# Performance work log

Hardware: AMD Instinct MI355X
Metric: run time of the kernel (lower is better)

## Reference

```python
import jax, jax.numpy as jnp
import numpy as np
from jax import lax

EPS = 1e-5

def _dsconv(x, dw, pw, g, b, m, v, relu):
    # x: [B,C,H,W]; dw: [C,1,3,3] depthwise; pw: [C,C,1,1] pointwise; eval-mode BN
    C = x.shape[1]
    y = lax.conv_general_dilated(x, dw, (1, 1), 'SAME', feature_group_count=C)
    y = lax.conv_general_dilated(y, pw, (1, 1), 'SAME')
    scale = (g * lax.rsqrt(v + EPS))[None, :, None, None]
    y = y * scale + (b - m * g * lax.rsqrt(v + EPS))[None, :, None, None]
    return jnp.maximum(y, 0.0) if relu else y

def _attention(x, wq, bq, wk, bk, wv, bv, gamma):
    b, c, h, w = x.shape
    n = h * w
    xf = x.reshape(b, c, n)                      # [B,C,N]
    q = jnp.einsum('oc,bcn->bon', wq, xf) + bq[None, :, None]   # [B,C/8,N]
    k = jnp.einsum('oc,bcn->bon', wk, xf) + bk[None, :, None]   # [B,C/8,N]
    v = jnp.einsum('oc,bcn->bon', wv, xf) + bv[None, :, None]   # [B,C,N]
    logits = jnp.einsum('bdm,bdn->bmn', q, k)    # q^T k, [B,N,N]
    attn = jax.nn.softmax(logits, axis=2)
    out = jnp.einsum('bcn,bmn->bcm', v, attn).reshape(b, c, h, w)
    return gamma[0] * out + x

def setup_inputs() -> dict:
    key = jax.random.key(0)
    ks = jax.random.split(key, 20)
    B, C, H, W = 64, 256, 32, 32
    C8 = C // 8
    rn = lambda k, s, sc: (jax.random.normal(k, s, dtype=jnp.float32) * sc)
    return {
        'x': rn(ks[0], (B, C, H, W), 1.0),
        'dw1': rn(ks[1], (C, 1, 3, 3), 0.2),
        'pw1': rn(ks[2], (C, C, 1, 1), 0.06),
        'bn1_g': jax.random.uniform(ks[3], (C,), jnp.float32, 0.5, 1.5),
        'bn1_b': rn(ks[4], (C,), 0.1),
        'bn1_m': rn(ks[5], (C,), 0.1),
        'bn1_v': jax.random.uniform(ks[6], (C,), jnp.float32, 0.5, 1.5),
        'dw2': rn(ks[7], (C, 1, 3, 3), 0.2),
        'pw2': rn(ks[8], (C, C, 1, 1), 0.06),
        'bn2_g': jax.random.uniform(ks[9], (C,), jnp.float32, 0.5, 1.5),
        'bn2_b': rn(ks[10], (C,), 0.1),
        'bn2_m': rn(ks[11], (C,), 0.1),
        'bn2_v': jax.random.uniform(ks[12], (C,), jnp.float32, 0.5, 1.5),
        'wq': rn(ks[13], (C8, C), 0.06),
        'bq': rn(ks[14], (C8,), 0.02),
        'wk': rn(ks[15], (C8, C), 0.06),
        'bk': rn(ks[16], (C8,), 0.02),
        'wv': rn(ks[17], (C, C), 0.06),
        'bv': rn(ks[18], (C,), 0.02),
        'gamma': rn(ks[19], (1,), 0.5),
    }

def reference(x, dw1, pw1, bn1_g, bn1_b, bn1_m, bn1_v,
              dw2, pw2, bn2_g, bn2_b, bn2_m, bn2_v,
              wq, bq, wk, bk, wv, bv, gamma):
    out = _dsconv(x, dw1, pw1, bn1_g, bn1_b, bn1_m, bn1_v, relu=True)
    out = _dsconv(out, dw2, pw2, bn2_g, bn2_b, bn2_m, bn2_v, relu=False)
    out = _attention(out + x, wq, bq, wk, bk, wv, bv, gamma)
    return jnp.maximum(out, 0.0)
```

## Files before the change

kernel.cpp:

```cpp
#include <hip/hip_runtime.h>
#include <cstdint>
#include <cstddef>

#define B_ 64
#define C_ 256
#define N_ 1024
#define LOG2E 1.4426950408889634f

typedef short v8s __attribute__((ext_vector_type(8)));
typedef float v4f __attribute__((ext_vector_type(4)));
typedef unsigned int u32;
typedef unsigned short u16;

__device__ __forceinline__ float bf2f(u16 u) {
  return __uint_as_float(((u32)u) << 16);
}
__device__ __forceinline__ u16 f2bf(float f) {
  u32 x = __float_as_uint(f);
  x += 0x7fffu + ((x >> 16) & 1u);
  return (u16)(x >> 16);
}
__device__ __forceinline__ u32 pack2(float a, float b) {
  return (u32)f2bf(a) | ((u32)f2bf(b) << 16);
}

typedef __attribute__((address_space(3))) unsigned int lds_as_t;
typedef __attribute__((address_space(1))) const unsigned int glb_as_t;
__device__ __forceinline__ void ld_lds16(const u16* g, u16* l) {
  __builtin_amdgcn_global_load_lds((glb_as_t*)g, (lds_as_t*)l, 16, 0, 0);
}

__global__ __launch_bounds__(256) void prep(
    const float* __restrict__ g1, const float* __restrict__ b1,
    const float* __restrict__ m1, const float* __restrict__ v1,
    const float* __restrict__ g2, const float* __restrict__ b2,
    const float* __restrict__ m2, const float* __restrict__ v2,
    const float* __restrict__ wq, const float* __restrict__ bq,
    const float* __restrict__ wk, const float* __restrict__ bk,
    const float* __restrict__ wv, const float* __restrict__ bv,
    const float* __restrict__ pw1, const float* __restrict__ pw2,
    const float* __restrict__ dw1, const float* __restrict__ dw2,
    float* __restrict__ scale1, float* __restrict__ shift1,
    float* __restrict__ scale2, float* __restrict__ shift2,
    float* __restrict__ dwT1, float* __restrict__ dwT2,
    u16* __restrict__ pw1b, u16* __restrict__ pw2b, u16* __restrict__ wcatb,
    float* __restrict__ bcat) {
  const int gt = blockIdx.x * 256 + threadIdx.x;
  if (gt < 256) {
    float s1 = g1[gt] * rsqrtf(v1[gt] + 1e-5f);
    scale1[gt] = s1;
    shift1[gt] = b1[gt] - m1[gt] * s1;
    float s2 = g2[gt] * rsqrtf(v2[gt] + 1e-5f);
    scale2[gt] = s2;
    shift2[gt] = b2[gt] - m2[gt] * s2;
  }
  if (gt < 320)
    bcat[gt] = (gt < 32) ? bq[gt] * LOG2E
                         : (gt < 64) ? bk[gt - 32] : bv[gt - 64];
  if (gt < 2304) {
    dwT1[(gt % 9) * 256 + gt / 9] = dw1[gt];
    dwT2[(gt % 9) * 256 + gt / 9] = dw2[gt];
  }
  for (int e = gt; e < 65536; e += 16384) {
    pw1b[e] = f2bf(pw1[e]);
    pw2b[e] = f2bf(pw2[e]);
  }
  for (int e = gt; e < 81920; e += 16384) {
    const int o = e >> 8;
    float w = (o < 32) ? wq[e] * LOG2E
                       : (o < 64) ? wk[e - 8192] : wv[e - 16384];
    wcatb[e] = f2bf(w);
  }
}

__global__ __launch_bounds__(256) void transpose_x(const float* __restrict__ x,
                                                   u16* __restrict__ xt) {
  __shared__ float t[64][65];
  const int b = blockIdx.z, c0 = blockIdx.y * 64, n0 = blockIdx.x * 64;
  const float* xp = x + ((size_t)b * C_ + c0) * N_ + n0;
  const int tn = threadIdx.x & 63, tc = threadIdx.x >> 6;
#pragma unroll
  for (int i = 0; i < 16; ++i)
    t[tc + 4 * i][tn] = xp[(size_t)(tc + 4 * i) * N_ + tn];
  __syncthreads();
  u16* op = xt + ((size_t)b * N_ + n0) * C_ + c0;
  const int oc = threadIdx.x & 63, on = threadIdx.x >> 6;
#pragma unroll
  for (int i = 0; i < 16; ++i)
    op[(size_t)(on + 4 * i) * C_ + oc] = f2bf(t[oc][on + 4 * i]);
}

__global__ __launch_bounds__(256) void dw_nhwc(const u16* __restrict__ src,
                                               const float* __restrict__ wT,
                                               u16* __restrict__ dst) {
  __shared__ float wl[9][256];
  const int b = blockIdx.y;
  for (int e = threadIdx.x; e < 2304; e += 256) wl[e >> 8][e & 255] = wT[e];
  __syncthreads();
  const int pl = threadIdx.x >> 5, c0 = (threadIdx.x & 31) * 8;
  const int p = blockIdx.x * 8 + pl;
  const int h = p >> 5, wx = p & 31;
  const u16* sp = src + (size_t)b * N_ * C_;
  float acc[8] = {0.f, 0.f, 0.f, 0.f, 0.f, 0.f, 0.f, 0.f};
#pragma unroll
  for (int dh = -1; dh <= 1; ++dh) {
    const int hh = h + dh;
    if (hh < 0 || hh > 31) continue;
#pragma unroll
    for (int dx = -1; dx <= 1; ++dx) {
      const int ww = wx + dx;
      if (ww < 0 || ww > 31) continue;
      const int k = (dh + 1) * 3 + (dx + 1);
      const uint4 v = *(const uint4*)(sp + (size_t)(hh * 32 + ww) * C_ + c0);
      const u32 vv[4] = {v.x, v.y, v.z, v.w};
#pragma unroll
      for (int j = 0; j < 4; ++j) {
        acc[2 * j] += bf2f((u16)(vv[j] & 0xffffu)) * wl[k][c0 + 2 * j];
        acc[2 * j + 1] += bf2f((u16)(vv[j] >> 16)) * wl[k][c0 + 2 * j + 1];
      }
    }
  }
  uint4 o4;
  o4.x = pack2(acc[0], acc[1]);
  o4.y = pack2(acc[2], acc[3]);
  o4.z = pack2(acc[4], acc[5]);
  o4.w = pack2(acc[6], acc[7]);
  *(uint4*)(dst + ((size_t)b * N_ + p) * C_ + c0) = o4;
}

template <int EPI>
__global__ __launch_bounds__(256) void gemm(
    const u16* __restrict__ X, const u16* __restrict__ W,
    const float* __restrict__ scale, const float* __restrict__ shift,
    const u16* __restrict__ resid, u16* __restrict__ Y, u16* __restrict__ Y2) {
  __shared__ u16 smem[17408];
  u16(*Xs)[64] = (u16(*)[64])smem;
  u16(*Ws)[64] = (u16(*)[64])(smem + 8192);
  u16(*Ys)[136] = (u16(*)[136])smem;
  u16(*YsQ)[68] = (u16(*)[68])smem;

  const int tid = threadIdx.x;
  const int b = blockIdx.z;
  const int n0 = blockIdx.x * 128, o0 = blockIdx.y * 128;
  const int wid = tid >> 6, lane = tid & 63;
  const int wn = wid & 1, wo = wid >> 1;
  const int l15 = lane & 15, l4 = lane >> 4;
  const int lr = lane >> 3, lc = (lane & 7) * 8;

  v4f acc[4][4];
#pragma unroll
  for (int i = 0; i < 4; ++i)
#pragma unroll
    for (int j = 0; j < 4; ++j) acc[i][j] = v4f{0.f, 0.f, 0.f, 0.f};

  for (int k0 = 0; k0 < C_; k0 += 64) {
#pragma unroll
    for (int g = 0; g < 4; ++g) {
      const int base = wid * 32 + g * 8;
      ld_lds16(X + ((size_t)b * N_ + n0 + base + lr) * C_ + k0 + lc,
               &Xs[base][0]);
      int wr = o0 + base + lr;
      if (EPI == 2 && wr > 319) wr = 319;
      ld_lds16(W + (size_t)wr * C_ + k0 + lc, &Ws[base][0]);
    }
    __syncthreads();
#pragma unroll
    for (int ks = 0; ks < 2; ++ks) {
      v8s af[4], bf4[4];
#pragma unroll
      for (int f = 0; f < 4; ++f) {
        if constexpr (EPI != 2) {
          af[f] = *(const v8s*)&Ws[wo * 64 + f * 16 + l15][ks * 32 + l4 * 8];
          bf4[f] = *(const v8s*)&Xs[wn * 64 + f * 16 + l15][ks * 32 + l4 * 8];
        } else {
          af[f] = *(const v8s*)&Xs[wn * 64 + f * 16 + l15][ks * 32 + l4 * 8];
          bf4[f] = *(const v8s*)&Ws[wo * 64 + f * 16 + l15][ks * 32 + l4 * 8];
        }
      }
#pragma unroll
      for (int i = 0; i < 4; ++i)
#pragma unroll
        for (int j = 0; j < 4; ++j)
          acc[i][j] = __builtin_amdgcn_mfma_f32_16x16x32_bf16(
              af[i], bf4[j], acc[i][j], 0, 0, 0);
    }
    __syncthreads();
  }

  if constexpr (EPI != 2) {
#pragma unroll
    for (int i = 0; i < 4; ++i) {
      const int oL = wo * 64 + i * 16 + l4 * 4;
      const int o = o0 + oL;
      const float4 sc = *(const float4*)&scale[o];
      const float4 sh = *(const float4*)&shift[o];
#pragma unroll
      for (int j = 0; j < 4; ++j) {
        const int nL = wn * 64 + j * 16 + l15;
        float y0 = acc[i][j][0] * sc.x + sh.x;
        float y1 = acc[i][j][1] * sc.y + sh.y;
        float y2 = acc[i][j][2] * sc.z + sh.z;
        float y3 = acc[i][j][3] * sc.w + sh.w;
        if constexpr (EPI == 0) {
          y0 = fmaxf(y0, 0.f);
          y1 = fmaxf(y1, 0.f);
          y2 = fmaxf(y2, 0.f);
          y3 = fmaxf(y3, 0.f);
        } else {
          const uint2 rb =
              *(const uint2*)(resid + ((size_t)b * N_ + n0 + nL) * C_ + o);
          y0 += bf2f((u16)(rb.x & 0xffffu));
          y1 += bf2f((u16)(rb.x >> 16));
          y2 += bf2f((u16)(rb.y & 0xffffu));
          y3 += bf2f((u16)(rb.y >> 16));
        }
        uint2 st;
        st.x = pack2(y0, y1);
        st.y = pack2(y2, y3);
        *(uint2*)&Ys[nL][oL] = st;
      }
    }
    __syncthreads();
#pragma unroll
    for (int s = 0; s < 8; ++s) {
      const int nL = s * 16 + (tid >> 4);
      const int slot = tid & 15;
      const uint4 v = *(const uint4*)&Ys[nL][slot * 8];
      *(uint4*)&Y[((size_t)b * N_ + n0 + nL) * C_ + o0 + slot * 8] = v;
    }
  } else {
    float bj[4];
#pragma unroll
    for (int j = 0; j < 4; ++j) {
      int o = o0 + wo * 64 + j * 16 + l15;
      bj[j] = shift[o > 319 ? 319 : o];
    }
    if (o0 == 0 && wo == 0) {
#pragma unroll
      for (int i = 0; i < 4; ++i) {
        const int nL = wn * 64 + i * 16 + l4 * 4;
#pragma unroll
        for (int j = 0; j < 4; ++j) {
          const int oL = j * 16 + l15;
#pragma unroll
          for (int r = 0; r < 4; ++r) YsQ[nL + r][oL] = f2bf(acc[i][j][r] + bj[j]);
        }
      }
    } else {
#pragma unroll
      for (int i = 0; i < 4; ++i) {
        const int nL = wn * 64 + i * 16 + l4 * 4;
#pragma unroll
        for (int j = 0; j < 4; ++j) {
          const int oL = wo * 64 + j * 16 + l15;
          uint2 st;
          st.x = pack2(acc[i][j][0] + bj[j], acc[i][j][1] + bj[j]);
          st.y = pack2(acc[i][j][2] + bj[j], acc[i][j][3] + bj[j]);
          *(uint2*)&Ys[oL][nL] = st;
        }
      }
    }
    __syncthreads();
    if (o0 == 0) {
#pragma unroll
      for (int s = 0; s < 4; ++s) {
        const int e = s * 256 + tid;
        const int row = e >> 3, seg = e & 7;
        const uint4 v = *(const uint4*)&YsQ[row][seg * 8];
        *(uint4*)&Y[((size_t)b * N_ + n0 + row) * 64 + seg * 8] = v;
      }
#pragma unroll
      for (int s = 0; s < 4; ++s) {
        const int e = s * 256 + tid;
        const int oL = 64 + (e >> 4), slot = e & 15;
        const uint4 v = *(const uint4*)&Ys[oL][slot * 8];
        *(uint4*)&Y2[((size_t)b * C_ + oL - 64) * N_ + n0 + slot * 8] = v;
      }
    } else {
#pragma unroll
      for (int s = 0; s < 8; ++s) {
        const int oL = s * 16 + (tid >> 4);
        const int c = o0 + oL - 64;
        if (c < 256) {
          const int slot = tid & 15;
          const uint4 v = *(const uint4*)&Ys[oL][slot * 8];
          *(uint4*)&Y2[((size_t)b * C_ + c) * N_ + n0 + slot * 8] = v;
        }
      }
    }
  }
}

__global__ __launch_bounds__(256, 3) void flash(
    const u16* __restrict__ qk, const u16* __restrict__ vchw,
    const u16* __restrict__ abf, const float* __restrict__ gamma_p,
    float* __restrict__ out) {
  const int b = blockIdx.x;
  const int m0 = blockIdx.y * 64;
  const int tid = threadIdx.x, wid = tid >> 6, lane = tid & 63;
  const int l15 = lane & 15, l4 = lane >> 4;
  const int mw = m0 + wid * 16;
  const int cq = wid * 64;

  __shared__ u16 Vs[256][64];
  __shared__ u16 Pl[2][64][72];
  __shared__ float Sl[64];

  const u16* qkb = qk + (size_t)b * N_ * 64;
  const u16* vb = vchw + (size_t)b * C_ * N_;
  const v8s qf = *(const v8s*)&qkb[(size_t)(mw + l15) * 64 + l4 * 8];

  const int s_row = lane >> 3;
  const int s_j = (lane & 7) ^ (s_row & 7);

#pragma unroll
  for (int g = 0; g < 8; ++g) {
    const int base = cq + g * 8;
    ld_lds16(vb + (size_t)(base + s_row) * N_ + s_j * 8, &Vs[base][0]);
  }

  float Mloc = -3e38f;
  {
    v8s kf[4];
#pragma unroll
    for (int f = 0; f < 4; ++f)
      kf[f] = *(const v8s*)&qkb[(size_t)(f * 16 + l15) * 64 + 32 + l4 * 8];
    for (int t = 0; t < 16; ++t) {
      v8s kn[4];
      if (t < 15) {
        const int n1 = (t + 1) * 64;
#pragma unroll
        for (int f = 0; f < 4; ++f)
          kn[f] =
              *(const v8s*)&qkb[(size_t)(n1 + f * 16 + l15) * 64 + 32 + l4 * 8];
      }
#pragma unroll
      for (int f = 0; f < 4; ++f) {
        const v4f lt = __builtin_amdgcn_mfma_f32_16x16x32_bf16(
            kf[f], qf, v4f{0.f, 0.f, 0.f, 0.f}, 0, 0, 0);
        Mloc = fmaxf(Mloc, fmaxf(fmaxf(lt[0], lt[1]), fmaxf(lt[2], lt[3])));
      }
      if (t < 15) {
#pragma unroll
        for (int f = 0; f < 4; ++f) kf[f] = kn[f];
      }
    }
  }
  Mloc = fmaxf(Mloc, __shfl_xor(Mloc, 16));
  Mloc = fmaxf(Mloc, __shfl_xor(Mloc, 32));
  const float M = Mloc;

  v4f acc[4][4];
#pragma unroll
  for (int mf = 0; mf < 4; ++mf)
#pragma unroll
    for (int j = 0; j < 4; ++j) acc[mf][j] = v4f{0.f, 0.f, 0.f, 0.f};
  float S0 = 0.f, S1 = 0.f, S2 = 0.f, S3 = 0.f;
  v8s kf[4];
#pragma unroll
  for (int f = 0; f < 4; ++f)
    kf[f] = *(const v8s*)&qkb[(size_t)(f * 16 + l15) * 64 + 32 + l4 * 8];
  __syncthreads();

  for (int t = 0; t < 16; ++t) {
    const int tb = t & 1;
    v4f lt[4];
#pragma unroll
    for (int f = 0; f < 4; ++f)
      lt[f] = __builtin_amdgcn_mfma_f32_16x16x32_bf16(
          kf[f], qf, v4f{0.f, 0.f, 0.f, 0.f}, 0, 0, 0);
#pragma unroll
    for (int f = 0; f < 4; ++f) {
      const float p0 = exp2f(lt[f][0] - M);
      const float p1 = exp2f(lt[f][1] - M);
      const float p2 = exp2f(lt[f][2] - M);
      const float p3 = exp2f(lt[f][3] - M);
      S0 += p0;
      S1 += p1;
      S2 += p2;
      S3 += p3;
      uint2 pw;
      pw.x = pack2(p0, p1);
      pw.y = pack2(p2, p3);
      *(uint2*)&Pl[tb][wid * 16 + l15][f * 16 + l4 * 4] = pw;
    }
    if (t < 15) {
      const int n1 = (t + 1) * 64;
#pragma unroll
      for (int f = 0; f < 4; ++f)
        kf[f] =
            *(const v8s*)&qkb[(size_t)(n1 + f * 16 + l15) * 64 + 32 + l4 * 8];
    }
    __syncthreads();
    __builtin_amdgcn_s_setprio(1);
#pragma unroll
    for (int ks = 0; ks < 2; ++ks) {
      v8s pa[4];
#pragma unroll
      for (int mf = 0; mf < 4; ++mf)
        pa[mf] = *(const v8s*)&Pl[tb][mf * 16 + l15][ks * 32 + l4 * 8];
#pragma unroll
      for (int j = 0; j < 4; ++j) {
        const int col = 8 * (((ks * 4) + l4) ^ (l15 & 7));
        const v8s vf = *(const v8s*)&Vs[cq + j * 16 + l15][col];
#pragma unroll
        for (int mf = 0; mf < 4; ++mf)
          acc[mf][j] = __builtin_amdgcn_mfma_f32_16x16x32_bf16(
              pa[mf], vf, acc[mf][j], 0, 0, 0);
      }
    }
    __builtin_amdgcn_s_setprio(0);
    __builtin_amdgcn_sched_barrier(0);
    if (t < 15) {
      const int n1 = (t + 1) * 64;
#pragma unroll
      for (int g = 0; g < 8; ++g) {
        const int base = cq + g * 8;
        ld_lds16(vb + (size_t)(base + s_row) * N_ + n1 + s_j * 8, &Vs[base][0]);
      }
    }
  }

  float S = (S0 + S1) + (S2 + S3);
  S += __shfl_xor(S, 16);
  S += __shfl_xor(S, 32);
  if (lane < 16) Sl[wid * 16 + lane] = 1.f / S;
  __syncthreads();

  const float gma = gamma_p[0];
  float invv[4][4];
#pragma unroll
  for (int mf = 0; mf < 4; ++mf)
#pragma unroll
    for (int r = 0; r < 4; ++r) invv[mf][r] = Sl[mf * 16 + l4 * 4 + r];

#pragma unroll
  for (int mf = 0; mf < 4; ++mf) {
    const int mb = m0 + mf * 16 + l4 * 4;
#pragma unroll
    for (int j = 0; j < 4; ++j) {
      const int c = cq + j * 16 + l15;
      float4 y;
      float* yp = (float*)&y;
#pragma unroll
      for (int r = 0; r < 4; ++r) {
        const float av = bf2f(abf[((size_t)b * N_ + mb + r) * C_ + c]);
        yp[r] = fmaxf(gma * acc[mf][j][r] * invv[mf][r] + av, 0.f);
      }
      *(float4*)&out[((size_t)b * C_ + c) * N_ + mb] = y;
    }
  }
}

extern "C" void kernel_launch(void* const* d_in, const int* in_sizes, int n_in,
                              void* d_out, int out_size, void* d_ws,
                              size_t ws_size, hipStream_t stream) {
  const float* x = (const float*)d_in[0];
  const float* dw1 = (const float*)d_in[1];
  const float* pw1 = (const float*)d_in[2];
  const float* bn1g = (const float*)d_in[3];
  const float* bn1b = (const float*)d_in[4];
  const float* bn1m = (const float*)d_in[5];
  const float* bn1v = (const float*)d_in[6];
  const float* dw2 = (const float*)d_in[7];
  const float* pw2 = (const float*)d_in[8];
  const float* bn2g = (const float*)d_in[9];
  const float* bn2b = (const float*)d_in[10];
  const float* bn2m = (const float*)d_in[11];
  const float* bn2v = (const float*)d_in[12];
  const float* wq = (const float*)d_in[13];
  const float* bq = (const float*)d_in[14];
  const float* wk = (const float*)d_in[15];
  const float* bk = (const float*)d_in[16];
  const float* wv = (const float*)d_in[17];
  const float* bv = (const float*)d_in[18];
  const float* gamma = (const float*)d_in[19];
  float* out = (float*)d_out;

  char* ws = (char*)d_ws;
  size_t off = 0;
  auto alloc = [&](size_t bytes) {
    void* p = ws + off;
    off += (bytes + 255) & ~(size_t)255;
    return p;
  };
  const size_t NE = (size_t)B_ * N_ * C_;

  u16* bufA = (u16*)alloc(NE * 2);
  u16* bufB = (u16*)alloc(NE * 2);
  u16* bufC = (u16*)alloc(NE * 2);
  u16* abf = (u16*)alloc(NE * 2);
  float* scale1 = (float*)alloc(256 * 4);
  float* shift1 = (float*)alloc(256 * 4);
  float* scale2 = (float*)alloc(256 * 4);
  float* shift2 = (float*)alloc(256 * 4);
  float* dwT1 = (float*)alloc(2304 * 4);
  float* dwT2 = (float*)alloc(2304 * 4);
  u16* pw1b = (u16*)alloc(65536 * 2);
  u16* pw2b = (u16*)alloc(65536 * 2);
  u16* wcatb = (u16*)alloc(81920 * 2);
  float* bcat = (float*)alloc(384 * 4);

  u16* xt = bufA;
  u16* t1 = bufB;
  u16* y1 = bufC;
  u16* t2 = bufB;
  u16* qkbuf = bufC;
  u16* vchw = bufA;

  prep<<<64, 256, 0, stream>>>(bn1g, bn1b, bn1m, bn1v, bn2g, bn2b, bn2m, bn2v,
                               wq, bq, wk, bk, wv, bv, pw1, pw2, dw1, dw2,
                               scale1, shift1, scale2, shift2, dwT1, dwT2,
                               pw1b, pw2b, wcatb, bcat);
  transpose_x<<<dim3(16, 4, B_), 256, 0, stream>>>(x, xt);
  dw_nhwc<<<dim3(128, B_), 256, 0, stream>>>(xt, dwT1, t1);
  gemm<0><<<dim3(8, 2, B_), 256, 0, stream>>>(t1, pw1b, scale1, shift1,
                                              nullptr, y1, nullptr);
  dw_nhwc<<<dim3(128, B_), 256, 0, stream>>>(y1, dwT2, t2);
  gemm<1><<<dim3(8, 2, B_), 256, 0, stream>>>(t2, pw2b, scale2, shift2, xt,
                                              abf, nullptr);
  gemm<2><<<dim3(8, 3, B_), 256, 0, stream>>>(abf, wcatb, nullptr, bcat,
                                              nullptr, qkbuf, vchw);
  flash<<<dim3(64, 16), 256, 0, stream>>>(qkbuf, vchw, abf, gamma, out);
}
```

Baseline: 256.9 us.

## Double-buffer GEMM K-loop and use manual waitcnt barriers in attention

The GEMM kernel now keeps two LDS buffers and prefetches the next K tile with global_load_lds while computing on the current one. It replaces __syncthreads with explicit vmcnt and lgkmcnt waits plus raw barriers. The attention loop gets the same treatment, loading K and V fragments unconditionally so the wait counts stay uniform, and it packs bf16 with the hardware v_cvt_pk_bf16_f32 instruction. The goal is to hide global load latency and cut barrier and conversion cost. The trade-offs are double the LDS per block (possible occupancy loss), redundant loads on the final iteration, and fragile hand-counted waitcnt values.

```diff
diff --git a/kernel.cpp b/kernel.cpp
--- a/kernel.cpp
+++ b/kernel.cpp
@@ -12,6 +12,11 @@
 typedef unsigned int u32;
 typedef unsigned short u16;
 
+#define VMCNT(N) asm volatile("s_waitcnt vmcnt(" #N ")" ::: "memory")
+#define LGKM0 asm volatile("s_waitcnt lgkmcnt(0)" ::: "memory")
+#define SBAR __builtin_amdgcn_s_barrier()
+#define SCHEDB __builtin_amdgcn_sched_barrier(0)
+
 __device__ __forceinline__ float bf2f(u16 u) {
   return __uint_as_float(((u32)u) << 16);
 }
@@ -22,6 +27,11 @@
 }
 __device__ __forceinline__ u32 pack2(float a, float b) {
   return (u32)f2bf(a) | ((u32)f2bf(b) << 16);
+}
+__device__ __forceinline__ u32 cvtpk(float lo, float hi) {
+  u32 r;
+  asm("v_cvt_pk_bf16_f32 %0, %1, %2" : "=v"(r) : "v"(lo), "v"(hi));
+  return r;
 }
 
 typedef __attribute__((address_space(3))) unsigned int lds_as_t;
@@ -133,9 +143,7 @@
     const u16* __restrict__ X, const u16* __restrict__ W,
     const float* __restrict__ scale, const float* __restrict__ shift,
     const u16* __restrict__ resid, u16* __restrict__ Y, u16* __restrict__ Y2) {
-  __shared__ u16 smem[17408];
-  u16(*Xs)[64] = (u16(*)[64])smem;
-  u16(*Ws)[64] = (u16(*)[64])(smem + 8192);
+  __shared__ u16 smem[32768];
   u16(*Ys)[136] = (u16(*)[136])smem;
   u16(*YsQ)[68] = (u16(*)[68])smem;
 
@@ -153,17 +161,36 @@
 #pragma unroll
     for (int j = 0; j < 4; ++j) acc[i][j] = v4f{0.f, 0.f, 0.f, 0.f};
 
-  for (int k0 = 0; k0 < C_; k0 += 64) {
+  auto stage = [&](int kidx, int bufsel) {
+    const int k0 = (kidx & 3) * 64;
+    u16* Xd = smem + bufsel * 16384;
+    u16* Wd = smem + bufsel * 16384 + 8192;
 #pragma unroll
     for (int g = 0; g < 4; ++g) {
       const int base = wid * 32 + g * 8;
       ld_lds16(X + ((size_t)b * N_ + n0 + base + lr) * C_ + k0 + lc,
-               &Xs[base][0]);
+               Xd + base * 64);
       int wr = o0 + base + lr;
       if (EPI == 2 && wr > 319) wr = 319;
-      ld_lds16(W + (size_t)wr * C_ + k0 + lc, &Ws[base][0]);
-    }
-    __syncthreads();
+      ld_lds16(W + (size_t)wr * C_ + k0 + lc, Wd + base * 64);
+    }
+  };
+
+  stage(0, 0);
+  stage(1, 1);
+
+#pragma unroll
+  for (int k = 0; k < 4; ++k) {
+    const int cur = k & 1;
+    if (k < 3) {
+      VMCNT(8);
+    } else {
+      VMCNT(0);
+    }
+    SCHEDB;
+    SBAR;
+    const u16(*Xs)[64] = (const u16(*)[64])(smem + cur * 16384);
+    const u16(*Ws)[64] = (const u16(*)[64])(smem + cur * 16384 + 8192);
 #pragma unroll
     for (int ks = 0; ks < 2; ++ks) {
       v8s af[4], bf4[4];
@@ -184,7 +211,10 @@
           acc[i][j] = __builtin_amdgcn_mfma_f32_16x16x32_bf16(
               af[i], bf4[j], acc[i][j], 0, 0, 0);
     }
-    __syncthreads();
+    LGKM0;
+    SBAR;
+    SCHEDB;
+    if (k < 2) stage(k + 2, cur);
   }
 
   if constexpr (EPI != 2) {
@@ -243,7 +273,8 @@
         for (int j = 0; j < 4; ++j) {
           const int oL = j * 16 + l15;
 #pragma unroll
-          for (int r = 0; r < 4; ++r) YsQ[nL + r][oL] = f2bf(acc[i][j][r] + bj[j]);
+          for (int r = 0; r < 4; ++r)
+            YsQ[nL + r][oL] = f2bf(acc[i][j][r] + bj[j]);
         }
       }
     } else {
@@ -360,7 +391,7 @@
 #pragma unroll
   for (int f = 0; f < 4; ++f)
     kf[f] = *(const v8s*)&qkb[(size_t)(f * 16 + l15) * 64 + 32 + l4 * 8];
-  __syncthreads();
+  VMCNT(0);
 
   for (int t = 0; t < 16; ++t) {
     const int tb = t & 1;
@@ -380,18 +411,23 @@
       S2 += p2;
       S3 += p3;
       uint2 pw;
-      pw.x = pack2(p0, p1);
-      pw.y = pack2(p2, p3);
+      pw.x = cvtpk(p0, p1);
+      pw.y = cvtpk(p2, p3);
       *(uint2*)&Pl[tb][wid * 16 + l15][f * 16 + l4 * 4] = pw;
     }
-    if (t < 15) {
-      const int n1 = (t + 1) * 64;
+    SCHEDB;
+    {
+      const int n1 = ((t + 1) & 15) * 64;
 #pragma unroll
       for (int f = 0; f < 4; ++f)
         kf[f] =
             *(const v8s*)&qkb[(size_t)(n1 + f * 16 + l15) * 64 + 32 + l4 * 8];
     }
-    __syncthreads();
+    SCHEDB;
+    LGKM0;
+    SBAR;
+    VMCNT(4);
+    SCHEDB;
     __builtin_amdgcn_s_setprio(1);
 #pragma unroll
     for (int ks = 0; ks < 2; ++ks) {
@@ -410,15 +446,16 @@
       }
     }
     __builtin_amdgcn_s_setprio(0);
-    __builtin_amdgcn_sched_barrier(0);
-    if (t < 15) {
-      const int n1 = (t + 1) * 64;
+    SCHEDB;
+    {
+      const int n1 = ((t + 1) & 15) * 64;
 #pragma unroll
       for (int g = 0; g < 8; ++g) {
         const int base = cq + g * 8;
         ld_lds16(vb + (size_t)(base + s_row) * N_ + n1 + s_j * 8, &Vs[base][0]);
       }
     }
+    SCHEDB;
   }
 
   float S = (S0 + S1) + (S2 + S3);
```

After: 256.3 us. Within noise of the previous version (-0.3%).
